# Optimization experiments

Measured on AMD Instinct MI355X. Metric: run time of the kernel, lower is better.

The kernel has to match this reference:

```python
import jax, jax.numpy as jnp
import numpy as np

P, L, D, H, K = 128, 800, 200, 100, 2  # passages, seq_len, input dim, hidden, spans per passage
VOCAB = 30522


def setup_inputs() -> dict:
    key = jax.random.key(0)
    ks = jax.random.split(key, 8)
    S_p = jax.random.normal(ks[0], (P, L, D), dtype=jnp.float32)
    # sorted along last axis so start <= end
    spans = jnp.sort(jax.random.randint(ks[1], (P, K, 2), 0, L), axis=-1)
    passages = jax.random.randint(ks[2], (P, L), 0, VOCAB)
    s = 0.05
    Wb = jax.random.normal(ks[3], (H, D), jnp.float32) * s
    We = jax.random.normal(ks[4], (H, D), jnp.float32) * s
    Wc = jax.random.normal(ks[5], (H, H), jnp.float32) * s
    Wo = jax.random.normal(ks[6], (H, H), jnp.float32) * s
    Wv = jax.random.normal(ks[7], (1, H), jnp.float32) * s
    return {"S_p": S_p, "spans": spans, "passages": passages,
            "Wb": Wb, "We": We, "Wc": Wc, "Wo": Wo, "Wv": Wv}


def reference(S_p, spans, passages, Wb, We, Wc, Wo, Wv):
    M = P * K
    p_idx = jnp.repeat(jnp.arange(P), K)            # [M] passage index per candidate
    starts = spans[:, :, 0].reshape(M)
    ends = spans[:, :, 1].reshape(M)
    t = jnp.arange(L)

    # S_Cs: candidate kept at its original position, zero elsewhere (== F.pad of the slice)
    span_mask = (t[None, :] >= starts[:, None]) & (t[None, :] <= ends[:, None])  # [M, L]
    S_Cs = S_p[p_idx] * span_mask[..., None].astype(S_p.dtype)                   # [M, L, D]

    # encoded candidates: token ids shifted to position 0, right-padded with 0
    gidx = jnp.clip(starts[:, None] + t[None, :], 0, L - 1)                      # [M, L]
    len_mask = t[None, :] <= (ends - starts)[:, None]
    encoded_candidates = jnp.where(len_mask, passages[p_idx[:, None], gidx], 0)  # [M, L]

    # condensed representation from start/end token states
    sb = S_p[p_idx, starts]                          # [M, D]
    se = S_p[p_idx, ends]                            # [M, D]
    r_Cs = jnp.tanh(sb @ Wb.T + se @ We.T)           # [M, H]

    # pairwise scores V_full[i, j] = Wv tanh(Wc r_i + Wo r_j)
    c = r_Cs @ Wc.T                                  # [M, H]
    o = r_Cs @ Wo.T                                  # [M, H]
    V_full = jnp.tanh(c[:, None, :] + o[None, :, :]) @ Wv[0]   # [M, M]

    # leave-one-out gather: V[i] = V_full[i, j != i]
    cols = jnp.arange(M - 1)
    rows = jnp.arange(M)
    idx = cols[None, :] + (cols[None, :] >= rows[:, None]).astype(cols.dtype)    # [M, M-1]
    V = V_full[rows[:, None], idx]                   # [M, M-1]

    # alpha[i] = exp(V[i]) / sum_{j != i} exp(V[j])  (per-column, non-standard normalization)
    E = jnp.exp(V)                                   # [M, M-1]
    denom = E.sum(axis=0, keepdims=True) - E
    alpha = E / denom                                # [M, M-1]

    # tilda_r[i] = sum over rows of (alpha excl row i) @ (r_Cs excl row i)
    s_rows = alpha.sum(axis=0, keepdims=True) - alpha   # [M, M-1]
    R_excl = r_Cs[idx]                                  # [M, M-1, H]
    tilda_r_Cs = jnp.einsum('mb,mbh->mh', s_rows, R_excl)  # [M, H]

    return S_Cs, r_Cs, encoded_candidates, V, tilda_r_Cs
```

## Files before the change

### kernel.cpp

```cpp
#include <hip/hip_runtime.h>
#include <math.h>

#define LP 800
#define DP 200
#define HP 100
#define MP 256
#define MM1 255

typedef float fx4 __attribute__((ext_vector_type(4)));

#define OFF_SCS  0u
#define OFF_R    40960000u
#define OFF_ENC  40985600u
#define OFF_V    41190400u
#define OFF_TIL  41255680u

#define WS_C     0u
#define WS_O     25600u
#define WS_S     51200u

#define SCS_TOTAL 5120
#define SCS_B1 1707
#define SCS_B2 1707
#define SCS_B3 1706
#define NB1 0
#define NB2 1707
#define NB3 3414

__device__ __forceinline__ float tanh_fast(float x) {
    float e = __expf(2.0f * x);
    return 1.0f - 2.0f / (e + 1.0f);
}

__device__ __forceinline__ void scs_slice(const fx4* __restrict__ Sp4,
                                          const int* __restrict__ spans,
                                          fx4* __restrict__ out4,
                                          unsigned sid) {
    unsigned m     = sid / 20u;
    unsigned chunk = sid - m * 20u;
    unsigned p = m >> 1, k = m & 1;
    int start = spans[p * 4 + k * 2];
    int end   = spans[p * 4 + k * 2 + 1];
    const fx4* __restrict__ src = Sp4 + (size_t)p * 40000u;
    fx4* __restrict__ dst       = out4 + (size_t)m * 40000u;
    unsigned base = chunk * 2048u + threadIdx.x;

    if (chunk < 19u) {
        fx4 v[8];
        #pragma unroll
        for (int it = 0; it < 8; ++it) {
            unsigned off = base + (unsigned)it * 256u;
            int t = (int)(off / 50u);
            fx4 x = (fx4)(0.f);
            if (t >= start && t <= end) x = src[off];
            v[it] = x;
        }
        #pragma unroll
        for (int it = 0; it < 8; ++it) {
            unsigned off = base + (unsigned)it * 256u;
            __builtin_nontemporal_store(v[it], &dst[off]);
        }
    } else {
        #pragma unroll
        for (int it = 0; it < 8; ++it) {
            unsigned off = base + (unsigned)it * 256u;
            if (off < 40000u) {
                int t = (int)(off / 50u);
                fx4 x = (fx4)(0.f);
                if (t >= start && t <= end) x = src[off];
                __builtin_nontemporal_store(x, &dst[off]);
            }
        }
    }
}

__global__ __launch_bounds__(256) void node1_kernel(const float* __restrict__ Sp,
                                                    const int* __restrict__ spans,
                                                    const int* __restrict__ passages,
                                                    const float* __restrict__ Wb,
                                                    const float* __restrict__ We,
                                                    const float* __restrict__ Wc,
                                                    const float* __restrict__ Wo,
                                                    float* __restrict__ enc,
                                                    float* __restrict__ r_out,
                                                    float* __restrict__ c_ws,
                                                    float* __restrict__ o_ws,
                                                    fx4* __restrict__ out4) {
    if (blockIdx.x >= MP) {
        scs_slice((const fx4*)Sp, spans, out4, NB1 + blockIdx.x - MP);
        return;
    }
    __shared__ float4 sb4[50], se4[50], rs4[25];
    int m = blockIdx.x;
    int p = m >> 1, k = m & 1;
    int start = spans[p * 4 + k * 2];
    int end   = spans[p * 4 + k * 2 + 1];
    int tid = threadIdx.x;

    int len = end - start;
    for (int t = tid; t < LP; t += 256) {
        int g = start + t; if (g > LP - 1) g = LP - 1;
        enc[m * LP + t] = (t <= len) ? (float)passages[p * LP + g] : 0.f;
    }

    const float4* sbp = (const float4*)(Sp + (size_t)(p * LP + start) * DP);
    const float4* sep = (const float4*)(Sp + (size_t)(p * LP + end) * DP);
    if (tid < 50)       sb4[tid]      = sbp[tid];
    else if (tid < 100) se4[tid - 50] = sep[tid - 50];
    __syncthreads();

    int h = tid;
    if (h < HP) {
        const float4* wb = (const float4*)(Wb + h * DP);
        const float4* we = (const float4*)(We + h * DP);
        float acc = 0.f;
        #pragma unroll
        for (int d = 0; d < 50; ++d) {
            float4 a = sb4[d], b = wb[d];
            acc += a.x * b.x + a.y * b.y + a.z * b.z + a.w * b.w;
            float4 a2 = se4[d], b2 = we[d];
            acc += a2.x * b2.x + a2.y * b2.y + a2.z * b2.z + a2.w * b2.w;
        }
        float r = tanh_fast(acc);
        ((float*)rs4)[h] = r;
        r_out[m * HP + h] = r;
    }
    __syncthreads();
    if (h < HP) {
        const float4* wc = (const float4*)(Wc + h * HP);
        const float4* wo = (const float4*)(Wo + h * HP);
        float accc = 0.f, acco = 0.f;
        #pragma unroll
        for (int q = 0; q < 25; ++q) {
            float4 r = rs4[q], cc = wc[q], oo = wo[q];
            accc += r.x * cc.x + r.y * cc.y + r.z * cc.z + r.w * cc.w;
            acco += r.x * oo.x + r.y * oo.y + r.z * oo.z + r.w * oo.w;
        }
        c_ws[m * HP + h] = accc;
        o_ws[m * HP + h] = acco;
    }
}

__global__ __launch_bounds__(256) void node2_kernel(const float* __restrict__ Sp,
                                                    const int* __restrict__ spans,
                                                    const float* __restrict__ c_ws,
                                                    const float* __restrict__ o_ws,
                                                    const float* __restrict__ Wv,
                                                    float* __restrict__ V_out,
                                                    float* __restrict__ s_ws,
                                                    fx4* __restrict__ out4) {
    if (blockIdx.x >= MM1) {
        scs_slice((const fx4*)Sp, spans, out4, NB2 + blockIdx.x - MM1);
        return;
    }
    __shared__ float4 olo4[25], ohi4[25], wv4[25];
    __shared__ float part[4];
    int jp = blockIdx.x;
    int i = threadIdx.x;
    if (i < 25) {
        olo4[i] = ((const float4*)(o_ws + jp * HP))[i];
        ohi4[i] = ((const float4*)(o_ws + (jp + 1) * HP))[i];
        wv4[i]  = ((const float4*)Wv)[i];
    }
    __syncthreads();

    const float4* c4p = (const float4*)(c_ws + i * HP);
    bool hi = (jp >= i);
    float acc = 0.f;
    #pragma unroll
    for (int q = 0; q < 25; ++q) {
        float4 c4 = c4p[q];
        float4 o4 = hi ? ohi4[q] : olo4[q];
        float4 w4 = wv4[q];
        acc += tanh_fast(c4.x + o4.x) * w4.x;
        acc += tanh_fast(c4.y + o4.y) * w4.y;
        acc += tanh_fast(c4.z + o4.z) * w4.z;
        acc += tanh_fast(c4.w + o4.w) * w4.w;
    }
    V_out[i * MM1 + jp] = acc;
    float e = __expf(acc);

    float v = e;
    v += __shfl_down(v, 32); v += __shfl_down(v, 16); v += __shfl_down(v, 8);
    v += __shfl_down(v, 4);  v += __shfl_down(v, 2);  v += __shfl_down(v, 1);
    if ((i & 63) == 0) part[i >> 6] = v;
    __syncthreads();
    float colE = part[0] + part[1] + part[2] + part[3];

    float a = e / (colE - e);

    __syncthreads();
    float v2 = a;
    v2 += __shfl_down(v2, 32); v2 += __shfl_down(v2, 16); v2 += __shfl_down(v2, 8);
    v2 += __shfl_down(v2, 4);  v2 += __shfl_down(v2, 2);  v2 += __shfl_down(v2, 1);
    if ((i & 63) == 0) part[i >> 6] = v2;
    __syncthreads();
    float colA = part[0] + part[1] + part[2] + part[3];

    s_ws[i * MM1 + jp] = colA - a;
}

__global__ __launch_bounds__(256) void node3_kernel(const float* __restrict__ Sp,
                                                    const int* __restrict__ spans,
                                                    const float* __restrict__ s_ws,
                                                    const float* __restrict__ r_out,
                                                    float* __restrict__ til_out,
                                                    fx4* __restrict__ out4) {
    if (blockIdx.x >= MP) {
        scs_slice((const fx4*)Sp, spans, out4, NB3 + blockIdx.x - MP);
        return;
    }
    __shared__ float s[MM1 + 1];
    int i = blockIdx.x;
    for (int jp = threadIdx.x; jp < MM1; jp += 256)
        s[jp] = s_ws[i * MM1 + jp];
    __syncthreads();
    int h = threadIdx.x;
    if (h < HP) {
        float acc = 0.f;
        #pragma unroll 4
        for (int jp = 0; jp < i; ++jp)
            acc += s[jp] * r_out[jp * HP + h];
        #pragma unroll 4
        for (int jp = i; jp < MM1; ++jp)
            acc += s[jp] * r_out[(jp + 1) * HP + h];
        til_out[i * HP + h] = acc;
    }
}

extern "C" void kernel_launch(void* const* d_in, const int* in_sizes, int n_in,
                              void* d_out, int out_size, void* d_ws, size_t ws_size,
                              hipStream_t stream) {
    const float* S_p      = (const float*)d_in[0];
    const int*   spans    = (const int*)d_in[1];
    const int*   passages = (const int*)d_in[2];
    const float* Wb       = (const float*)d_in[3];
    const float* We       = (const float*)d_in[4];
    const float* Wc       = (const float*)d_in[5];
    const float* Wo       = (const float*)d_in[6];
    const float* Wv       = (const float*)d_in[7];

    float* out = (float*)d_out;
    float* ws  = (float*)d_ws;

    float* out_scs = out + OFF_SCS;
    float* out_r   = out + OFF_R;
    float* out_enc = out + OFF_ENC;
    float* out_v   = out + OFF_V;
    float* out_til = out + OFF_TIL;

    float* ws_c = ws + WS_C;
    float* ws_o = ws + WS_O;
    float* ws_s = ws + WS_S;

    fx4* out4 = (fx4*)out_scs;

    node1_kernel<<<MP + SCS_B1, 256, 0, stream>>>(S_p, spans, passages,
                                                  Wb, We, Wc, Wo,
                                                  out_enc, out_r, ws_c, ws_o, out4);
    node2_kernel<<<MM1 + SCS_B2, 256, 0, stream>>>(S_p, spans, ws_c, ws_o, Wv,
                                                   out_v, ws_s, out4);
    node3_kernel<<<MP + SCS_B3, 256, 0, stream>>>(S_p, spans, ws_s, out_r,
                                                  out_til, out4);
}
```

Measured before the change: 273.4 us.

## Fuse three stage kernels into one cooperative persistent kernel with grid syncs

```diff
diff --git a/kernel.cpp b/kernel.cpp
--- a/kernel.cpp
+++ b/kernel.cpp
@@ -1,5 +1,8 @@
 #include <hip/hip_runtime.h>
+#include <hip/hip_cooperative_groups.h>
 #include <math.h>
+
+namespace cg = cooperative_groups;
 
 #define LP 800
 #define DP 200
@@ -20,6 +23,12 @@
 #define WS_S     51200u
 
 #define SCS_TOTAL 5120
+
+#define GRID  1024
+#define PRE_A (GRID - MP)
+#define PRE_B (GRID - MM1)
+#define REM   (SCS_TOTAL - PRE_A - PRE_B)
+
 #define SCS_B1 1707
 #define SCS_B2 1707
 #define SCS_B3 1706
@@ -72,6 +81,160 @@
             }
         }
     }
+}
+
+__global__ __launch_bounds__(256, 4) void fused_kernel(
+        const float* __restrict__ Sp,
+        const int* __restrict__ spans,
+        const int* __restrict__ passages,
+        const float* __restrict__ Wb,
+        const float* __restrict__ We,
+        const float* __restrict__ Wc,
+        const float* __restrict__ Wo,
+        const float* __restrict__ Wv,
+        float* __restrict__ enc,
+        float* __restrict__ r_out,
+        float* __restrict__ V_out,
+        float* __restrict__ til_out,
+        float* __restrict__ c_ws,
+        float* __restrict__ o_ws,
+        float* __restrict__ s_ws,
+        fx4* __restrict__ out4) {
+    __shared__ float4 sb4[50], se4[50], rs4[25];
+    __shared__ float4 olo4[25], ohi4[25], wv4[25];
+    __shared__ float part[4];
+    __shared__ float srow[MM1 + 1];
+
+    cg::grid_group grid = cg::this_grid();
+    const int bid = blockIdx.x;
+    const int tid = threadIdx.x;
+
+    if (bid < MP) {
+        int m = bid;
+        int p = m >> 1, k = m & 1;
+        int start = spans[p * 4 + k * 2];
+        int end   = spans[p * 4 + k * 2 + 1];
+
+        int len = end - start;
+        for (int t = tid; t < LP; t += 256) {
+            int g = start + t; if (g > LP - 1) g = LP - 1;
+            enc[m * LP + t] = (t <= len) ? (float)passages[p * LP + g] : 0.f;
+        }
+
+        const float4* sbp = (const float4*)(Sp + (size_t)(p * LP + start) * DP);
+        const float4* sep = (const float4*)(Sp + (size_t)(p * LP + end) * DP);
+        if (tid < 50)       sb4[tid]      = sbp[tid];
+        else if (tid < 100) se4[tid - 50] = sep[tid - 50];
+        __syncthreads();
+
+        int h = tid;
+        if (h < HP) {
+            const float4* wb = (const float4*)(Wb + h * DP);
+            const float4* we = (const float4*)(We + h * DP);
+            float acc = 0.f;
+            #pragma unroll
+            for (int d = 0; d < 50; ++d) {
+                float4 a = sb4[d], b = wb[d];
+                acc += a.x * b.x + a.y * b.y + a.z * b.z + a.w * b.w;
+                float4 a2 = se4[d], b2 = we[d];
+                acc += a2.x * b2.x + a2.y * b2.y + a2.z * b2.z + a2.w * b2.w;
+            }
+            float r = tanh_fast(acc);
+            ((float*)rs4)[h] = r;
+            r_out[m * HP + h] = r;
+        }
+        __syncthreads();
+        if (h < HP) {
+            const float4* wc = (const float4*)(Wc + h * HP);
+            const float4* wo = (const float4*)(Wo + h * HP);
+            float accc = 0.f, acco = 0.f;
+            #pragma unroll
+            for (int q = 0; q < 25; ++q) {
+                float4 r = rs4[q], cc = wc[q], oo = wo[q];
+                accc += r.x * cc.x + r.y * cc.y + r.z * cc.z + r.w * cc.w;
+                acco += r.x * oo.x + r.y * oo.y + r.z * oo.z + r.w * oo.w;
+            }
+            c_ws[m * HP + h] = accc;
+            o_ws[m * HP + h] = acco;
+        }
+    } else {
+        scs_slice((const fx4*)Sp, spans, out4,
+                  (unsigned)(SCS_TOTAL - 1) - (unsigned)(bid - MP));
+    }
+    __threadfence();
+    grid.sync();
+
+    if (bid < MM1) {
+        int jp = bid;
+        int i = tid;
+        if (i < 25) {
+            olo4[i] = ((const float4*)(o_ws + jp * HP))[i];
+            ohi4[i] = ((const float4*)(o_ws + (jp + 1) * HP))[i];
+            wv4[i]  = ((const float4*)Wv)[i];
+        }
+        __syncthreads();
+
+        const float4* c4p = (const float4*)(c_ws + i * HP);
+        bool hi = (jp >= i);
+        float acc = 0.f;
+        #pragma unroll
+        for (int q = 0; q < 25; ++q) {
+            float4 c4 = c4p[q];
+            float4 o4 = hi ? ohi4[q] : olo4[q];
+            float4 w4 = wv4[q];
+            acc += tanh_fast(c4.x + o4.x) * w4.x;
+            acc += tanh_fast(c4.y + o4.y) * w4.y;
+            acc += tanh_fast(c4.z + o4.z) * w4.z;
+            acc += tanh_fast(c4.w + o4.w) * w4.w;
+        }
+        V_out[i * MM1 + jp] = acc;
+        float e = __expf(acc);
+
+        float v = e;
+        v += __shfl_down(v, 32); v += __shfl_down(v, 16); v += __shfl_down(v, 8);
+        v += __shfl_down(v, 4);  v += __shfl_down(v, 2);  v += __shfl_down(v, 1);
+        if ((i & 63) == 0) part[i >> 6] = v;
+        __syncthreads();
+        float colE = part[0] + part[1] + part[2] + part[3];
+
+        float a = e / (colE - e);
+
+        __syncthreads();
+        float v2 = a;
+        v2 += __shfl_down(v2, 32); v2 += __shfl_down(v2, 16); v2 += __shfl_down(v2, 8);
+        v2 += __shfl_down(v2, 4);  v2 += __shfl_down(v2, 2);  v2 += __shfl_down(v2, 1);
+        if ((i & 63) == 0) part[i >> 6] = v2;
+        __syncthreads();
+        float colA = part[0] + part[1] + part[2] + part[3];
+
+        s_ws[i * MM1 + jp] = colA - a;
+    } else {
+        scs_slice((const fx4*)Sp, spans, out4,
+                  (unsigned)(SCS_TOTAL - PRE_A - 1) - (unsigned)(bid - MM1));
+    }
+    __threadfence();
+    grid.sync();
+
+    if (bid < MP) {
+        int i = bid;
+        for (int jp = tid; jp < MM1; jp += 256)
+            srow[jp] = s_ws[i * MM1 + jp];
+        __syncthreads();
+        int h = tid;
+        if (h < HP) {
+            float acc = 0.f;
+            #pragma unroll 4
+            for (int jp = 0; jp < i; ++jp)
+                acc += srow[jp] * r_out[jp * HP + h];
+            #pragma unroll 4
+            for (int jp = i; jp < MM1; ++jp)
+                acc += srow[jp] * r_out[(jp + 1) * HP + h];
+            til_out[i * HP + h] = acc;
+        }
+    }
+
+    for (unsigned sid = (unsigned)bid; sid < (unsigned)REM; sid += (unsigned)GRID)
+        scs_slice((const fx4*)Sp, spans, out4, sid);
 }
 
 __global__ __launch_bounds__(256) void node1_kernel(const float* __restrict__ Sp,
@@ -255,11 +418,22 @@
 
     fx4* out4 = (fx4*)out_scs;
 
-    node1_kernel<<<MP + SCS_B1, 256, 0, stream>>>(S_p, spans, passages,
-                                                  Wb, We, Wc, Wo,
-                                                  out_enc, out_r, ws_c, ws_o, out4);
-    node2_kernel<<<MM1 + SCS_B2, 256, 0, stream>>>(S_p, spans, ws_c, ws_o, Wv,
-                                                   out_v, ws_s, out4);
-    node3_kernel<<<MP + SCS_B3, 256, 0, stream>>>(S_p, spans, ws_s, out_r,
-                                                  out_til, out4);
-}
+    void* args[] = {
+        (void*)&S_p, (void*)&spans, (void*)&passages,
+        (void*)&Wb, (void*)&We, (void*)&Wc, (void*)&Wo, (void*)&Wv,
+        (void*)&out_enc, (void*)&out_r, (void*)&out_v, (void*)&out_til,
+        (void*)&ws_c, (void*)&ws_o, (void*)&ws_s, (void*)&out4
+    };
+    hipError_t err = hipLaunchCooperativeKernel((const void*)fused_kernel,
+                                                dim3(GRID), dim3(256),
+                                                args, 0, stream);
+    if (err != hipSuccess) {
+        node1_kernel<<<MP + SCS_B1, 256, 0, stream>>>(S_p, spans, passages,
+                                                      Wb, We, Wc, Wo,
+                                                      out_enc, out_r, ws_c, ws_o, out4);
+        node2_kernel<<<MM1 + SCS_B2, 256, 0, stream>>>(S_p, spans, ws_c, ws_o, Wv,
+                                                       out_v, ws_s, out4);
+        node3_kernel<<<MP + SCS_B3, 256, 0, stream>>>(S_p, spans, ws_s, out_r,
+                                                      out_til, out4);
+    }
+}
```

After: 742.5 us. 172% more time.
